# Optimization experiments

Measured on AMD Instinct MI355X. Metric: run time of the kernel, lower is better.

The kernel has to match this reference:

```python
import jax, jax.numpy as jnp
import numpy as np

HIDDEN = 2048
N_HEADS = 16
N_KV_HEADS = 4
HEAD_DIM = HIDDEN // N_HEADS  # 128
WINDOW = 2048
ROPE_THETA = 10000.0


def setup_inputs() -> dict:
    key = jax.random.key(0)
    ks = jax.random.split(key, 5)
    B, S = 1, 4096
    scale = 0.02
    return {
        "hidden_states": jax.random.normal(ks[0], (B, S, HIDDEN), dtype=jnp.float32),
        # nn.Linear weights are [out_features, in_features]
        "q_w": jax.random.normal(ks[1], (N_HEADS * HEAD_DIM, HIDDEN), dtype=jnp.float32) * scale,
        "k_w": jax.random.normal(ks[2], (N_KV_HEADS * HEAD_DIM, HIDDEN), dtype=jnp.float32) * scale,
        "v_w": jax.random.normal(ks[3], (N_KV_HEADS * HEAD_DIM, HIDDEN), dtype=jnp.float32) * scale,
        "o_w": jax.random.normal(ks[4], (HIDDEN, N_HEADS * HEAD_DIM), dtype=jnp.float32) * scale,
    }


def _rope_cos_sin(seq_len, dtype):
    inv_freq = 1.0 / (ROPE_THETA ** (jnp.arange(0, HEAD_DIM, 2, dtype=jnp.float32) / HEAD_DIM))
    pos = jnp.arange(seq_len, dtype=jnp.float32)
    freqs = pos[:, None] * inv_freq[None, :]          # [S, D/2]
    emb = jnp.concatenate([freqs, freqs], axis=-1)    # [S, D]
    return jnp.cos(emb).astype(dtype), jnp.sin(emb).astype(dtype)


def _rotate_half(x):
    x1, x2 = jnp.split(x, 2, axis=-1)
    return jnp.concatenate([-x2, x1], axis=-1)


def reference(hidden_states, q_w, k_w, v_w, o_w):
    B, S, _ = hidden_states.shape
    dtype = hidden_states.dtype

    q = hidden_states @ q_w.T                         # [B,S,H*D]
    k = hidden_states @ k_w.T                         # [B,S,Hkv*D]
    v = hidden_states @ v_w.T

    q = q.reshape(B, S, N_HEADS, HEAD_DIM).transpose(0, 2, 1, 3)      # [B,H,S,D]
    k = k.reshape(B, S, N_KV_HEADS, HEAD_DIM).transpose(0, 2, 1, 3)   # [B,Hkv,S,D]
    v = v.reshape(B, S, N_KV_HEADS, HEAD_DIM).transpose(0, 2, 1, 3)

    cos, sin = _rope_cos_sin(S, dtype)                # [S,D]
    cos = cos[None, None]
    sin = sin[None, None]
    q = q * cos + _rotate_half(q) * sin
    k = k * cos + _rotate_half(k) * sin

    n_rep = N_HEADS // N_KV_HEADS
    k = jnp.repeat(k, n_rep, axis=1)                  # [B,H,S,D]
    v = jnp.repeat(v, n_rep, axis=1)

    scores = jnp.einsum("bhqd,bhkd->bhqk", q, k) / jnp.sqrt(jnp.array(HEAD_DIM, dtype))

    pos = jnp.arange(S)
    rel = pos[:, None] - pos[None, :]
    allowed = (rel >= 0) & (rel < WINDOW)             # causal sliding window
    mask = jnp.where(allowed, jnp.array(0.0, dtype), jnp.array(-jnp.inf, dtype))
    scores = scores + mask[None, None]

    attn = jax.nn.softmax(scores.astype(jnp.float32), axis=-1).astype(dtype)

    out = jnp.einsum("bhqk,bhkd->bhqd", attn, v)      # [B,H,S,D]
    out = out.transpose(0, 2, 1, 3).reshape(B, S, N_HEADS * HEAD_DIM)
    return out @ o_w.T
```

## Files before the change

kernel.cpp:

```cpp
#include <hip/hip_runtime.h>
#include <stdint.h>

typedef unsigned short u16;
typedef unsigned int u32;
typedef float f32x4 __attribute__((ext_vector_type(4)));
typedef float f32x8 __attribute__((ext_vector_type(8)));
typedef int   i32x4 __attribute__((ext_vector_type(4)));
typedef __bf16 bf16x8 __attribute__((ext_vector_type(8)));
typedef u16 u16x4 __attribute__((ext_vector_type(4)));

constexpr int S_LEN = 4096;
constexpr int HID   = 2048;
constexpr int WIN   = 2048;

__device__ __forceinline__ u32 f2bf_u(float f) {
  u32 u = __builtin_bit_cast(u32, f);
  return (u + 0x7fffu + ((u >> 16) & 1u)) >> 16;
}
__device__ __forceinline__ float bf2f(u16 u) {
  return __builtin_bit_cast(float, ((u32)u) << 16);
}
__device__ __forceinline__ float exp2x(float x) {
#if __has_builtin(__builtin_amdgcn_exp2f)
  return __builtin_amdgcn_exp2f(x);
#else
  return exp2f(x);
#endif
}
__device__ __forceinline__ void mfma16(f32x4& acc, i32x4 a, i32x4 b) {
  acc = __builtin_amdgcn_mfma_f32_16x16x32_bf16(
      __builtin_bit_cast(bf16x8, a), __builtin_bit_cast(bf16x8, b), acc, 0, 0, 0);
}
__device__ __forceinline__ void gload_lds16(const u16* g, u16* l) {
  __builtin_amdgcn_global_load_lds((const __attribute__((address_space(1))) u32*)g,
                                   (__attribute__((address_space(3))) u32*)l, 16, 0, 0);
}

constexpr int CVT_B0 = 1048576;
constexpr int CVT_B1 = CVT_B0 + 524288;
constexpr int CVT_B2 = CVT_B1 + 131072;
constexpr int CVT_B3 = CVT_B2 + 131072;
constexpr int CVT_B4 = CVT_B3 + 524288;
constexpr int CVT_B5 = CVT_B4 + 32768;

__global__ __launch_bounds__(256) void cvt_all_kernel(
    const float* __restrict__ s0, const float* __restrict__ s1,
    const float* __restrict__ s2, const float* __restrict__ s3,
    const float* __restrict__ s4, u16* __restrict__ d0, u16* __restrict__ d1,
    u16* __restrict__ d2, u16* __restrict__ d3, u16* __restrict__ d4,
    float* __restrict__ cs, float* __restrict__ sn) {
  int t = blockIdx.x * 256 + threadIdx.x;
  if (t >= CVT_B4) {
    if (t >= CVT_B5) return;
    int e = (t - CVT_B4) * 8;
    int d = e & 63, s = e >> 6;
#pragma unroll
    for (int j = 0; j < 8; ++j) {
      float inv = exp2f(-(float)(d + j) * 0.20762050593046014f);
      float f = (float)s * inv;
      cs[e + j] = cosf(f);
      sn[e + j] = sinf(f);
    }
    return;
  }
  const float* s;
  u16* d;
  int off;
  if (t < CVT_B0) { s = s0; d = d0; off = t; }
  else if (t < CVT_B1) { s = s1; d = d1; off = t - CVT_B0; }
  else if (t < CVT_B2) { s = s2; d = d2; off = t - CVT_B1; }
  else if (t < CVT_B3) { s = s3; d = d3; off = t - CVT_B2; }
  else { s = s4; d = d4; off = t - CVT_B3; }
  const f32x4* sp = (const f32x4*)s + (size_t)off * 2;
  f32x4 a = sp[0], b = sp[1];
  i32x4 o;
  o.x = (int)(f2bf_u(a.x) | (f2bf_u(a.y) << 16));
  o.y = (int)(f2bf_u(a.z) | (f2bf_u(a.w) << 16));
  o.z = (int)(f2bf_u(b.x) | (f2bf_u(b.y) << 16));
  o.w = (int)(f2bf_u(b.z) | (f2bf_u(b.w) << 16));
  *((i32x4*)d + off) = o;
}

__global__ __launch_bounds__(256) void rope_qk_kernel(u16* __restrict__ Qb,
                                                      u16* __restrict__ Kb,
                                                      const float* __restrict__ cs,
                                                      const float* __restrict__ sn) {
  const float SC2 = 0.088388347648318447f * 1.4426950408889634f;
  int t = blockIdx.x * 256 + threadIdx.x;
  int d0 = (t & 15) * 4;
  int r = t >> 4;
  u16* p;
  int s;
  float qs;
  if (r < S_LEN * 16) {
    int h = r & 15; s = r >> 4;
    p = Qb + (size_t)s * HID + h * 128 + d0;
    qs = SC2;
  } else {
    int r2 = r - S_LEN * 16;
    int h = r2 & 3; s = r2 >> 2;
    p = Kb + (size_t)s * 512 + h * 128 + d0;
    qs = 1.f;
  }
  f32x4 c = *(const f32x4*)&cs[(s << 6) | d0];
  f32x4 si = *(const f32x4*)&sn[(s << 6) | d0];
  u16x4 a = *(u16x4*)p, b = *(u16x4*)(p + 64);
  u16x4 oa, ob;
#pragma unroll
  for (int j = 0; j < 4; ++j) {
    float x1 = bf2f(a[j]), x2 = bf2f(b[j]);
    oa[j] = (u16)f2bf_u((x1 * c[j] - x2 * si[j]) * qs);
    ob[j] = (u16)f2bf_u((x2 * c[j] + x1 * si[j]) * qs);
  }
  *(u16x4*)p = oa;
  *(u16x4*)(p + 64) = ob;
}

__device__ __forceinline__ void gemm256_core(const u16* __restrict__ A_,
                                             const u16* __restrict__ Bm_,
                                             int brow_, int bc_,
                                             f32x4 (&acc)[4][4], int& orow0,
                                             int& ocol0) {
  __shared__ __attribute__((aligned(16))) u16 sA[2][256 * 64];
  __shared__ __attribute__((aligned(16))) u16 sB[2][128 * 64];
  const int t = threadIdx.x;
  const int lane = t & 63;
  const int w = t >> 6;
  const int g = lane >> 4, ln = lane & 15;
  const int wm = w >> 1, wn = w & 1;
  const int trow = t >> 3, tslot = t & 7;
  const int sslot = tslot ^ (trow & 7);
  const u16* Abase = A_ + (size_t)(brow_ + trow) * 2048 + sslot * 8;
  const u16* Bbase = Bm_ + (size_t)(bc_ + trow) * 2048 + sslot * 8;

#define STAGE6(buf, kt)                                                        \
  {                                                                            \
    const int _k0 = (kt) * 64;                                                 \
    _Pragma("unroll") for (int a2 = 0; a2 < 4; ++a2)                           \
        gload_lds16(Abase + (size_t)a2 * 64 * 2048 + _k0,                      \
                    &sA[buf][a2 * 4096 + t * 8]);                              \
    _Pragma("unroll") for (int b2 = 0; b2 < 2; ++b2)                           \
        gload_lds16(Bbase + (size_t)b2 * 64 * 2048 + _k0,                      \
                    &sB[buf][b2 * 4096 + t * 8]);                              \
  }

  STAGE6(0, 0);
  STAGE6(1, 1);
  asm volatile("s_waitcnt vmcnt(6)" ::: "memory");
  __builtin_amdgcn_s_barrier();
  int cur = 0;
  for (int kt = 0; kt < 32; ++kt) {
    i32x4 bfr[4][2];
#pragma unroll
    for (int n = 0; n < 4; ++n) {
      const int row = wn * 64 + n * 16 + ln;
      const int sw = row & 7;
      bfr[n][0] = *(const i32x4*)&sB[cur][row * 64 + ((g ^ sw) << 3)];
      bfr[n][1] = *(const i32x4*)&sB[cur][row * 64 + (((4 | g) ^ sw) << 3)];
    }
    __builtin_amdgcn_s_setprio(1);
#pragma unroll
    for (int m = 0; m < 4; ++m) {
      const int row = wm * 64 + m * 16 + ln;
      const int sw = row & 7;
      i32x4 a0 = *(const i32x4*)&sA[cur][row * 64 + ((g ^ sw) << 3)];
      i32x4 a1 = *(const i32x4*)&sA[cur][row * 64 + (((4 | g) ^ sw) << 3)];
#pragma unroll
      for (int n = 0; n < 4; ++n) {
        mfma16(acc[m][n], a0, bfr[n][0]);
        mfma16(acc[m][n], a1, bfr[n][1]);
      }
    }
    __builtin_amdgcn_s_setprio(0);
    __builtin_amdgcn_s_barrier();
    if (kt + 2 < 32) {
      STAGE6(cur, kt + 2);
      asm volatile("s_waitcnt vmcnt(6)" ::: "memory");
    } else if (kt + 1 < 32) {
      asm volatile("s_waitcnt vmcnt(0)" ::: "memory");
    }
    __builtin_amdgcn_s_barrier();
    cur ^= 1;
  }
#undef STAGE6
  orow0 = brow_ + wm * 64 + g * 4;
  ocol0 = bc_ + wn * 64 + ln;
}

__global__ __launch_bounds__(512) void qkv256_kernel(
    const u16* __restrict__ A, const u16* __restrict__ Wq,
    const u16* __restrict__ Wk, const u16* __restrict__ Wv,
    u16* __restrict__ Qb, u16* __restrict__ Kb, u16* __restrict__ Vt) {
  int wgid = blockIdx.x;
  wgid = (wgid & 7) * 48 + (wgid >> 3);
  const int brow = (wgid / 24) * 256;
  const int bcol = (wgid % 24) * 128;
  const u16* Bm;
  u16* out;
  int bc, mode, N;
  if (bcol < 2048)      { Bm = Wq; out = Qb; bc = bcol;        N = 2048; mode = 0; }
  else if (bcol < 2560) { Bm = Wk; out = Kb; bc = bcol - 2048; N = 512;  mode = 0; }
  else                  { Bm = Wv; out = Vt; bc = bcol - 2560; N = 512;  mode = 1; }

  f32x4 acc[4][4] = {};
  int orow0, ocol0;
  gemm256_core(A, Bm, brow, bc, acc, orow0, ocol0);

#pragma unroll
  for (int m = 0; m < 4; ++m)
#pragma unroll
    for (int n = 0; n < 4; ++n)
#pragma unroll
      for (int j = 0; j < 4; ++j) {
        int row = orow0 + m * 16 + j;
        int col = ocol0 + n * 16;
        float v = acc[m][n][j];
        if (mode == 0) {
          out[(size_t)row * N + col] = (u16)f2bf_u(v);
        } else {
          int d = col & 127, kvh = col >> 7;
          int T = row >> 5, ks = row & 31;
          int tt = ks >> 4, gg = (ks >> 2) & 3, e = (tt << 2) | (ks & 3);
          size_t idx = (size_t)kvh * S_LEN * 128 + (size_t)T * 4096 +
                       (size_t)d * 32 + ((size_t)(gg ^ ((d >> 1) & 3)) << 3) + e;
          out[idx] = (u16)f2bf_u(v);
        }
      }
}

__global__ __launch_bounds__(512) void o256_kernel(const u16* __restrict__ A,
                                                   const u16* __restrict__ Bw,
                                                   float* __restrict__ Cv) {
  int wgid = blockIdx.x;
  wgid = (wgid & 7) * 32 + (wgid >> 3);
  const int brow = (wgid / 16) * 256;
  const int bcol = (wgid % 16) * 128;

  f32x4 acc[4][4] = {};
  int orow0, ocol0;
  gemm256_core(A, Bw, brow, bcol, acc, orow0, ocol0);

#pragma unroll
  for (int m = 0; m < 4; ++m)
#pragma unroll
    for (int n = 0; n < 4; ++n)
#pragma unroll
      for (int j = 0; j < 4; ++j)
        Cv[(size_t)(orow0 + m * 16 + j) * 2048 + ocol0 + n * 16] = acc[m][n][j];
}

__global__ __launch_bounds__(64) void attn_kernel(const u16* __restrict__ Q,
                                                  const u16* __restrict__ Kb,
                                                  const u16* __restrict__ Vt,
                                                  u16* __restrict__ opart,
                                                  float* __restrict__ mpart,
                                                  float* __restrict__ lpart) {
  const int lane = threadIdx.x;
  const int g = lane >> 4, ln = lane & 15;

  const int o = blockIdx.x;
  const int wgid = ((o & 7) << 9) | (o >> 3);
  const int h = wgid >> 8;
  const int idx = wgid & 255;
  const int chunk = idx & 1;
  const int gq = 127 - (idx >> 1);
  const int kvh = h >> 2;
  const int qr0 = gq * 32;

  i32x4 aq[2][4];
#pragma unroll
  for (int qf = 0; qf < 2; ++qf) {
    const u16* qp = Q + (size_t)(qr0 + qf * 16 + ln) * HID + h * 128 + g * 8;
#pragma unroll
    for (int c = 0; c < 4; ++c) aq[qf][c] = *(const i32x4*)(qp + c * 32);
  }

  f32x4 oacc[2][8] = {};
  float mrun[2] = {-1e30f, -1e30f};
  float lrun[2] = {0.f, 0.f};

  int lo = qr0 - (WIN - 1);
  if (lo < 0) lo = 0;
  lo &= ~31;
  const int nt_full = ((qr0 + 32) - lo) >> 5;
  const int nt0 = nt_full >> 1;
  const int lo_c = lo + (chunk ? nt0 * 32 : 0);
  const int nt = chunk ? nt_full - nt0 : nt0;

  const u16* kptr = Kb + (size_t)(lo_c + ln) * 512 + kvh * 128 + g * 8;
  const int vswz = (g ^ ((ln >> 1) & 3)) << 3;
  const u16* vptr = Vt + (size_t)kvh * S_LEN * 128 +
                    (size_t)(lo_c >> 5) * 4096 + ln * 32 + vswz;

  i32x4 kf[2][4], vf[8];
  if (nt > 0) {
#pragma unroll
    for (int tt = 0; tt < 2; ++tt)
#pragma unroll
      for (int c = 0; c < 4; ++c)
        kf[tt][c] = *(const i32x4*)(kptr + tt * 8192 + c * 32);
#pragma unroll
    for (int nf = 0; nf < 8; ++nf) vf[nf] = *(const i32x4*)(vptr + nf * 512);
  }

  for (int it = 0; it < nt; ++it) {
    const int kb = lo_c + it * 32;
    const bool more = (it + 1 < nt);

    f32x4 sc[2][2] = {};
    __builtin_amdgcn_s_setprio(1);
#pragma unroll
    for (int c = 0; c < 4; ++c) {
      mfma16(sc[0][0], kf[0][c], aq[0][c]);
      mfma16(sc[0][1], kf[1][c], aq[0][c]);
      mfma16(sc[1][0], kf[0][c], aq[1][c]);
      mfma16(sc[1][1], kf[1][c], aq[1][c]);
    }
    __builtin_amdgcn_s_setprio(0);

    if (more) {
      kptr += 32 * 512;
#pragma unroll
      for (int tt = 0; tt < 2; ++tt)
#pragma unroll
        for (int c = 0; c < 4; ++c)
          kf[tt][c] = *(const i32x4*)(kptr + tt * 8192 + c * 32);
    }

    float p[2][8];
    float mx[2];
    const bool interior = (kb + 31 <= qr0) && (qr0 + 31 - kb < WIN);
#pragma unroll
    for (int qf = 0; qf < 2; ++qf) {
      if (interior) {
#pragma unroll
        for (int j = 0; j < 4; ++j) {
          p[qf][j] = sc[qf][0][j];
          p[qf][4 + j] = sc[qf][1][j];
        }
      } else {
        const float NEG = -__builtin_inff();
        const int q = qr0 + qf * 16 + ln;
#pragma unroll
        for (int tt = 0; tt < 2; ++tt)
#pragma unroll
          for (int j = 0; j < 4; ++j) {
            int k = kb + tt * 16 + g * 4 + j;
            p[qf][tt * 4 + j] = (k <= q && q - k < WIN) ? sc[qf][tt][j] : NEG;
          }
      }
      float x0 = fmaxf(fmaxf(p[qf][0], p[qf][1]), p[qf][2]);
      float x1 = fmaxf(fmaxf(p[qf][3], p[qf][4]), p[qf][5]);
      float x2 = fmaxf(fmaxf(p[qf][6], p[qf][7]), x0);
      float m = fmaxf(x1, x2);
      m = fmaxf(m, __shfl_xor(m, 16));
      m = fmaxf(m, __shfl_xor(m, 32));
      mx[qf] = m;
    }

    float corr[2] = {1.f, 1.f};
    const bool noskip =
        !__all((mx[0] - mrun[0] <= 11.f) && (mx[1] - mrun[1] <= 11.f));
    if (noskip) {
#pragma unroll
      for (int qf = 0; qf < 2; ++qf) {
        float mnew = fmaxf(mrun[qf], mx[qf]);
        corr[qf] = exp2x(mrun[qf] - mnew);
        mrun[qf] = mnew;
        f32x4 cv;
#pragma unroll
        for (int j = 0; j < 4; ++j) cv[j] = __shfl(corr[qf], g * 4 + j);
#pragma unroll
        for (int nf = 0; nf < 8; ++nf)
#pragma unroll
          for (int j = 0; j < 4; ++j) oacc[qf][nf][j] *= cv[j];
      }
    }

    i32x4 pa[2];
#pragma unroll
    for (int qf = 0; qf < 2; ++qf) {
      f32x8 pv;
#pragma unroll
      for (int e = 0; e < 8; ++e) pv[e] = exp2x(p[qf][e] - mrun[qf]);
      float rs = ((pv[0] + pv[1]) + (pv[2] + pv[3])) +
                 ((pv[4] + pv[5]) + (pv[6] + pv[7]));
      lrun[qf] = lrun[qf] * corr[qf] + rs;
      bf16x8 pb = __builtin_convertvector(pv, bf16x8);
      pa[qf] = __builtin_bit_cast(i32x4, pb);
    }

    __builtin_amdgcn_s_setprio(1);
#pragma unroll
    for (int nf = 0; nf < 8; ++nf) {
      mfma16(oacc[0][nf], pa[0], vf[nf]);
      mfma16(oacc[1][nf], pa[1], vf[nf]);
    }
    __builtin_amdgcn_s_setprio(0);

    if (more) {
      vptr += 4096;
#pragma unroll
      for (int nf = 0; nf < 8; ++nf) vf[nf] = *(const i32x4*)(vptr + nf * 512);
    }
  }

#pragma unroll
  for (int qf = 0; qf < 2; ++qf) {
    float l = lrun[qf];
    l += __shfl_xor(l, 16);
    l += __shfl_xor(l, 32);
    lrun[qf] = l;
  }

  const size_t pb = ((size_t)chunk * 16 + h) * S_LEN;
#pragma unroll
  for (int qf = 0; qf < 2; ++qf) {
    if (g == 0) {
      mpart[pb + qr0 + qf * 16 + ln] = mrun[qf];
      lpart[pb + qr0 + qf * 16 + ln] = lrun[qf];
    }
    u16* aop = opart + (pb + qr0 + qf * 16 + g * 4) * 128 + ln;
#pragma unroll
    for (int j = 0; j < 4; ++j)
#pragma unroll
      for (int nf = 0; nf < 8; ++nf)
        aop[(size_t)j * 128 + nf * 16] = (u16)f2bf_u(oacc[qf][nf][j]);
  }
}

__global__ __launch_bounds__(256) void attn_combine_kernel(
    const u16* __restrict__ opart, const float* __restrict__ mpart,
    const float* __restrict__ lpart, u16* __restrict__ AO) {
  int t = blockIdx.x * 256 + threadIdx.x;
  int d0 = (t & 15) * 8;
  int rh = t >> 4;
  int row = rh & (S_LEN - 1);
  int h = rh >> 12;
  size_t i0 = (size_t)h * S_LEN + row;
  size_t i1 = i0 + (size_t)16 * S_LEN;
  float m0 = mpart[i0], m1 = mpart[i1];
  float l0 = lpart[i0], l1 = lpart[i1];
  float m = fmaxf(m0, m1);
  float w0 = exp2x(m0 - m), w1 = exp2x(m1 - m);
  float inv = 1.f / (l0 * w0 + l1 * w1);
  w0 *= inv;
  w1 *= inv;
  i32x4 v0 = *(const i32x4*)(opart + i0 * 128 + d0);
  i32x4 v1 = *(const i32x4*)(opart + i1 * 128 + d0);
  i32x4 ov;
#pragma unroll
  for (int j = 0; j < 4; ++j) {
    u32 a = ((u32)v0[j]), b = ((u32)v1[j]);
    float x = bf2f((u16)a) * w0 + bf2f((u16)b) * w1;
    float y = bf2f((u16)(a >> 16)) * w0 + bf2f((u16)(b >> 16)) * w1;
    ov[j] = (int)(f2bf_u(x) | (f2bf_u(y) << 16));
  }
  *(i32x4*)(AO + (size_t)row * HID + h * 128 + d0) = ov;
}

extern "C" void kernel_launch(void* const* d_in, const int* in_sizes, int n_in,
                              void* d_out, int out_size, void* d_ws, size_t ws_size,
                              hipStream_t stream) {
  const float* hx = (const float*)d_in[0];
  const float* qw = (const float*)d_in[1];
  const float* kw = (const float*)d_in[2];
  const float* vw = (const float*)d_in[3];
  const float* ow = (const float*)d_in[4];

  char* p = (char*)d_ws;
  u16* Xb = (u16*)p; p += (size_t)S_LEN * HID * 2;
  u16* Wq = (u16*)p; p += (size_t)HID * HID * 2;
  u16* Wk = (u16*)p; p += (size_t)512 * HID * 2;
  u16* Wv = (u16*)p; p += (size_t)512 * HID * 2;
  u16* Wo = (u16*)p; p += (size_t)HID * HID * 2;
  u16* Qb = (u16*)p; p += (size_t)S_LEN * HID * 2;
  u16* Kb = (u16*)p; p += (size_t)S_LEN * 512 * 2;
  u16* Vt = (u16*)p; p += (size_t)S_LEN * 512 * 2;
  u16* AO = (u16*)p; p += (size_t)S_LEN * HID * 2;
  float* cs = (float*)p; p += (size_t)S_LEN * 64 * 4;
  float* sn = (float*)p; p += (size_t)S_LEN * 64 * 4;
  u16* Opart = (u16*)p; p += (size_t)2 * 16 * S_LEN * 128 * 2;
  float* Mpart = (float*)p; p += (size_t)2 * 16 * S_LEN * 4;
  float* Lpart = (float*)p; p += (size_t)2 * 16 * S_LEN * 4;

  cvt_all_kernel<<<(CVT_B5 + 255) / 256, 256, 0, stream>>>(
      hx, qw, kw, vw, ow, Xb, Wq, Wk, Wv, Wo, cs, sn);

  qkv256_kernel<<<384, 512, 0, stream>>>(Xb, Wq, Wk, Wv, Qb, Kb, Vt);

  rope_qk_kernel<<<S_LEN * 20 * 16 / 256, 256, 0, stream>>>(Qb, Kb, cs, sn);

  attn_kernel<<<4096, 64, 0, stream>>>(Qb, Kb, Vt, Opart, Mpart, Lpart);
  attn_combine_kernel<<<S_LEN * 16 * 16 / 256, 256, 0, stream>>>(Opart, Mpart,
                                                                 Lpart, AO);

  o256_kernel<<<256, 512, 0, stream>>>(AO, Wo, (float*)d_out);
}
```

Baseline: 298.0 us.

## Fuse split-KV combine into attention kernel using last-arriver atomic flags

Removes the separate attn_combine launch. Each attention workgroup now publishes its partial result, fences, and bumps a per-(head, query-block) atomic counter. The second of the two chunk workgroups to finish reads both partials and writes the merged bf16 output directly. This saves one kernel launch and its gap, in exchange for a memset, atomics and fences, and a serial combine tail inside the last workgroup.

```diff
diff --git a/kernel.cpp b/kernel.cpp
--- a/kernel.cpp
+++ b/kernel.cpp
@@ -254,7 +254,9 @@
                                                   const u16* __restrict__ Vt,
                                                   u16* __restrict__ opart,
                                                   float* __restrict__ mpart,
-                                                  float* __restrict__ lpart) {
+                                                  float* __restrict__ lpart,
+                                                  u32* __restrict__ flags,
+                                                  u16* __restrict__ AO) {
   const int lane = threadIdx.x;
   const int g = lane >> 4, ln = lane & 15;
 
@@ -427,36 +429,42 @@
       for (int nf = 0; nf < 8; ++nf)
         aop[(size_t)j * 128 + nf * 16] = (u16)f2bf_u(oacc[qf][nf][j]);
   }
-}
-
-__global__ __launch_bounds__(256) void attn_combine_kernel(
-    const u16* __restrict__ opart, const float* __restrict__ mpart,
-    const float* __restrict__ lpart, u16* __restrict__ AO) {
-  int t = blockIdx.x * 256 + threadIdx.x;
-  int d0 = (t & 15) * 8;
-  int rh = t >> 4;
-  int row = rh & (S_LEN - 1);
-  int h = rh >> 12;
-  size_t i0 = (size_t)h * S_LEN + row;
-  size_t i1 = i0 + (size_t)16 * S_LEN;
-  float m0 = mpart[i0], m1 = mpart[i1];
-  float l0 = lpart[i0], l1 = lpart[i1];
-  float m = fmaxf(m0, m1);
-  float w0 = exp2x(m0 - m), w1 = exp2x(m1 - m);
-  float inv = 1.f / (l0 * w0 + l1 * w1);
-  w0 *= inv;
-  w1 *= inv;
-  i32x4 v0 = *(const i32x4*)(opart + i0 * 128 + d0);
-  i32x4 v1 = *(const i32x4*)(opart + i1 * 128 + d0);
-  i32x4 ov;
-#pragma unroll
-  for (int j = 0; j < 4; ++j) {
-    u32 a = ((u32)v0[j]), b = ((u32)v1[j]);
-    float x = bf2f((u16)a) * w0 + bf2f((u16)b) * w1;
-    float y = bf2f((u16)(a >> 16)) * w0 + bf2f((u16)(b >> 16)) * w1;
-    ov[j] = (int)(f2bf_u(x) | (f2bf_u(y) << 16));
-  }
-  *(i32x4*)(AO + (size_t)row * HID + h * 128 + d0) = ov;
+
+  __threadfence();
+  u32 old = 0;
+  if (lane == 0) old = atomicAdd(&flags[(h << 7) | gq], 1u);
+  old = __shfl(old, 0);
+  if (old == 1) {
+    __threadfence();
+    const int row = qr0 + (lane >> 1);
+    const int dbase = (lane & 1) << 6;
+    const size_t r0 = (size_t)h * S_LEN + row;
+    const size_t r1 = r0 + (size_t)16 * S_LEN;
+    float m0 = mpart[r0], m1 = mpart[r1];
+    float l0 = lpart[r0], l1 = lpart[r1];
+    float m = fmaxf(m0, m1);
+    float w0 = exp2x(m0 - m), w1 = exp2x(m1 - m);
+    float inv = 1.f / (l0 * w0 + l1 * w1);
+    w0 *= inv;
+    w1 *= inv;
+    const u16* p0 = opart + r0 * 128 + dbase;
+    const u16* p1 = opart + r1 * 128 + dbase;
+    u16* ao = AO + (size_t)row * HID + h * 128 + dbase;
+#pragma unroll
+    for (int e = 0; e < 8; ++e) {
+      i32x4 v0 = *(const i32x4*)(p0 + e * 8);
+      i32x4 v1 = *(const i32x4*)(p1 + e * 8);
+      i32x4 ov;
+#pragma unroll
+      for (int j = 0; j < 4; ++j) {
+        u32 a = (u32)v0[j], b2 = (u32)v1[j];
+        float x = bf2f((u16)a) * w0 + bf2f((u16)b2) * w1;
+        float y = bf2f((u16)(a >> 16)) * w0 + bf2f((u16)(b2 >> 16)) * w1;
+        ov[j] = (int)(f2bf_u(x) | (f2bf_u(y) << 16));
+      }
+      *(i32x4*)(ao + e * 8) = ov;
+    }
+  }
 }
 
 extern "C" void kernel_launch(void* const* d_in, const int* in_sizes, int n_in,
@@ -483,6 +491,9 @@
   u16* Opart = (u16*)p; p += (size_t)2 * 16 * S_LEN * 128 * 2;
   float* Mpart = (float*)p; p += (size_t)2 * 16 * S_LEN * 4;
   float* Lpart = (float*)p; p += (size_t)2 * 16 * S_LEN * 4;
+  u32* Flags = (u32*)p; p += (size_t)16 * 128 * 4;
+
+  hipMemsetAsync(Flags, 0, 16 * 128 * 4, stream);
 
   cvt_all_kernel<<<(CVT_B5 + 255) / 256, 256, 0, stream>>>(
       hx, qw, kw, vw, ow, Xb, Wq, Wk, Wv, Wo, cs, sn);
@@ -491,9 +502,8 @@
 
   rope_qk_kernel<<<S_LEN * 20 * 16 / 256, 256, 0, stream>>>(Qb, Kb, cs, sn);
 
-  attn_kernel<<<4096, 64, 0, stream>>>(Qb, Kb, Vt, Opart, Mpart, Lpart);
-  attn_combine_kernel<<<S_LEN * 16 * 16 / 256, 256, 0, stream>>>(Opart, Mpart,
-                                                                 Lpart, AO);
+  attn_kernel<<<4096, 64, 0, stream>>>(Qb, Kb, Vt, Opart, Mpart, Lpart, Flags,
+                                       AO);
 
   o256_kernel<<<256, 512, 0, stream>>>(AO, Wo, (float*)d_out);
 }
```

Measured after the change: 496.8 us. +66.7%, slower.

## Split attention KV range into four chunks and remap workgroup ordering

Applied to the files above, without the earlier changes.

Raises the split-KV factor for the sliding-window attention from two to four chunks per query tile, doubling the grid to 8192 single-wave workgroups, and remaps block indices so neighbouring heads and chunks of the same query tile are scheduled together. The combine kernel now merges four partial results using their max and sum statistics. The aim is more parallelism and shorter per-wave loops to fill the GPU. The cost is twice the partial-output traffic and a heavier combine pass.

```diff
diff --git a/kernel.cpp b/kernel.cpp
--- a/kernel.cpp
+++ b/kernel.cpp
@@ -259,11 +259,11 @@
   const int g = lane >> 4, ln = lane & 15;
 
   const int o = blockIdx.x;
-  const int wgid = ((o & 7) << 9) | (o >> 3);
-  const int h = wgid >> 8;
-  const int idx = wgid & 255;
-  const int chunk = idx & 1;
-  const int gq = 127 - (idx >> 1);
+  const int r = o >> 3;
+  const int gq = 127 - (r >> 3);
+  const int sub = r & 7;
+  const int chunk = sub >> 1;
+  const int h = ((o & 7) << 1) | (sub & 1);
   const int kvh = h >> 2;
   const int qr0 = gq * 32;
 
@@ -283,9 +283,10 @@
   if (lo < 0) lo = 0;
   lo &= ~31;
   const int nt_full = ((qr0 + 32) - lo) >> 5;
-  const int nt0 = nt_full >> 1;
-  const int lo_c = lo + (chunk ? nt0 * 32 : 0);
-  const int nt = chunk ? nt_full - nt0 : nt0;
+  const int base = nt_full >> 2, rem = nt_full & 3;
+  const int nt = base + (chunk < rem ? 1 : 0);
+  const int start = chunk * base + (chunk < rem ? chunk : rem);
+  const int lo_c = lo + start * 32;
 
   const u16* kptr = Kb + (size_t)(lo_c + ln) * 512 + kvh * 128 + g * 8;
   const int vswz = (g ^ ((ln >> 1) & 3)) << 3;
@@ -438,24 +439,39 @@
   int row = rh & (S_LEN - 1);
   int h = rh >> 12;
   size_t i0 = (size_t)h * S_LEN + row;
-  size_t i1 = i0 + (size_t)16 * S_LEN;
-  float m0 = mpart[i0], m1 = mpart[i1];
-  float l0 = lpart[i0], l1 = lpart[i1];
-  float m = fmaxf(m0, m1);
-  float w0 = exp2x(m0 - m), w1 = exp2x(m1 - m);
-  float inv = 1.f / (l0 * w0 + l1 * w1);
-  w0 *= inv;
-  w1 *= inv;
-  i32x4 v0 = *(const i32x4*)(opart + i0 * 128 + d0);
-  i32x4 v1 = *(const i32x4*)(opart + i1 * 128 + d0);
+  const size_t cstride = (size_t)16 * S_LEN;
+  float mv[4], lv[4];
+#pragma unroll
+  for (int c = 0; c < 4; ++c) {
+    mv[c] = mpart[i0 + c * cstride];
+    lv[c] = lpart[i0 + c * cstride];
+  }
+  float m = fmaxf(fmaxf(mv[0], mv[1]), fmaxf(mv[2], mv[3]));
+  float wv[4], denom = 0.f;
+#pragma unroll
+  for (int c = 0; c < 4; ++c) {
+    wv[c] = exp2x(mv[c] - m);
+    denom += lv[c] * wv[c];
+  }
+  float inv = 1.f / denom;
+#pragma unroll
+  for (int c = 0; c < 4; ++c) wv[c] *= inv;
+
+  f32x8 accv = {};
+#pragma unroll
+  for (int c = 0; c < 4; ++c) {
+    i32x4 v = *(const i32x4*)(opart + (i0 + c * cstride) * 128 + d0);
+#pragma unroll
+    for (int j = 0; j < 4; ++j) {
+      u32 a = (u32)v[j];
+      accv[j * 2] += bf2f((u16)a) * wv[c];
+      accv[j * 2 + 1] += bf2f((u16)(a >> 16)) * wv[c];
+    }
+  }
   i32x4 ov;
 #pragma unroll
-  for (int j = 0; j < 4; ++j) {
-    u32 a = ((u32)v0[j]), b = ((u32)v1[j]);
-    float x = bf2f((u16)a) * w0 + bf2f((u16)b) * w1;
-    float y = bf2f((u16)(a >> 16)) * w0 + bf2f((u16)(b >> 16)) * w1;
-    ov[j] = (int)(f2bf_u(x) | (f2bf_u(y) << 16));
-  }
+  for (int j = 0; j < 4; ++j)
+    ov[j] = (int)(f2bf_u(accv[j * 2]) | (f2bf_u(accv[j * 2 + 1]) << 16));
   *(i32x4*)(AO + (size_t)row * HID + h * 128 + d0) = ov;
 }
 
@@ -480,9 +496,9 @@
   u16* AO = (u16*)p; p += (size_t)S_LEN * HID * 2;
   float* cs = (float*)p; p += (size_t)S_LEN * 64 * 4;
   float* sn = (float*)p; p += (size_t)S_LEN * 64 * 4;
-  u16* Opart = (u16*)p; p += (size_t)2 * 16 * S_LEN * 128 * 2;
-  float* Mpart = (float*)p; p += (size_t)2 * 16 * S_LEN * 4;
-  float* Lpart = (float*)p; p += (size_t)2 * 16 * S_LEN * 4;
+  u16* Opart = (u16*)p; p += (size_t)4 * 16 * S_LEN * 128 * 2;
+  float* Mpart = (float*)p; p += (size_t)4 * 16 * S_LEN * 4;
+  float* Lpart = (float*)p; p += (size_t)4 * 16 * S_LEN * 4;
 
   cvt_all_kernel<<<(CVT_B5 + 255) / 256, 256, 0, stream>>>(
       hx, qw, kw, vw, ow, Xb, Wq, Wk, Wv, Wo, cs, sn);
@@ -491,7 +507,7 @@
 
   rope_qk_kernel<<<S_LEN * 20 * 16 / 256, 256, 0, stream>>>(Qb, Kb, cs, sn);
 
-  attn_kernel<<<4096, 64, 0, stream>>>(Qb, Kb, Vt, Opart, Mpart, Lpart);
+  attn_kernel<<<8192, 64, 0, stream>>>(Qb, Kb, Vt, Opart, Mpart, Lpart);
   attn_combine_kernel<<<S_LEN * 16 * 16 / 256, 256, 0, stream>>>(Opart, Mpart,
                                                                  Lpart, AO);
 
```

Measured after the change: 312.3 us. 4.8% more time.
